# Kernel tuning notes

Measured on AMD Instinct MI355X. Metric: run time of the kernel, lower is better.

## Reference

```python
import jax, jax.numpy as jnp
import numpy as np

B, S, D, HD = 16, 2048, 1024, 64  # batch, seq, n_embd, head_dim


def setup_inputs() -> dict:
    key = jax.random.key(0)
    ks = jax.random.split(key, 4)
    std = 1.0 / np.sqrt(D)
    return {
        "x": jax.random.normal(ks[0], (B, S, D), dtype=jnp.float32),
        "Wq": jax.random.normal(ks[1], (D, HD), dtype=jnp.float32) * std,
        "bq": jnp.zeros((HD,), dtype=jnp.float32),
        "Wk": jax.random.normal(ks[2], (D, HD), dtype=jnp.float32) * std,
        "bk": jnp.zeros((HD,), dtype=jnp.float32),
        "Wv": jax.random.normal(ks[3], (D, HD), dtype=jnp.float32) * std,
        "bv": jnp.zeros((HD,), dtype=jnp.float32),
    }


def reference(x, Wq, bq, Wk, bk, Wv, bv):
    q = x @ Wq + bq  # [B,S,HD]
    k = x @ Wk + bk
    v = x @ Wv + bv
    scale = jnp.asarray(HD, x.dtype) ** -0.5
    scores = jnp.einsum("bqd,bkd->bqk", q, k) * scale  # [B,S,S]
    seq = x.shape[1]
    causal = jnp.tril(jnp.ones((seq, seq), dtype=bool))  # True = keep
    scores = jnp.where(causal, scores, jnp.asarray(-jnp.inf, scores.dtype))
    probs = jax.nn.softmax(scores, axis=-1)
    return jnp.einsum("bqk,bkd->bqd", probs, v)  # [B,S,HD]
```

## Files before the change

### kernel.cpp

```cpp
#include <hip/hip_runtime.h>
#include <hip/hip_bf16.h>
#include <math.h>

constexpr int Bsz  = 16;
constexpr int Seq  = 2048;
constexpr int Din  = 1024;
constexpr int Hd   = 64;
constexpr int Rows = Bsz * Seq;

typedef short  short8 __attribute__((ext_vector_type(8)));
typedef float  f32x4  __attribute__((ext_vector_type(4)));

__device__ __forceinline__ short bf16_bits(float f) {
    __hip_bfloat16 h = __float2bfloat16(f);
    return __builtin_bit_cast(short, h);
}

typedef __attribute__((address_space(1))) const void gvoid_t;
typedef __attribute__((address_space(3))) void lvoid_t;
__device__ __forceinline__ void gll16(const void* g, void* l) {
    __builtin_amdgcn_global_load_lds((gvoid_t*)g, (lvoid_t*)l, 16, 0, 0);
}

__global__ __launch_bounds__(256) void wt_prep(
    const float* __restrict__ Wq, const float* __restrict__ Wk,
    const float* __restrict__ Wv, short* __restrict__ Wf)
{
    const int u     = blockIdx.x * 256 + threadIdx.x;
    const int chunk = u / 768;
    const int rem   = u - chunk * 768;
    const int f     = rem >> 6;
    const int lane  = rem & 63;
    const int wg    = f >> 2, nt = f & 3;
    const int quad  = lane >> 4, l16 = lane & 15;
    const float* W  = (wg == 0) ? Wq : (wg == 1) ? Wk : Wv;
    const int k0 = chunk * 32 + quad * 8;
    const int n  = nt * 16 + l16;
    short8 v;
    #pragma unroll
    for (int j = 0; j < 8; ++j) v[j] = bf16_bits(W[(size_t)(k0 + j) * Hd + n]);
    *(short8*)(Wf + (size_t)u * 8) = v;
}

template<int RD, int ST, bool STAGE, bool PREF>
__device__ __forceinline__ void qkv_step(
    const short*& wf_stage, short* sW, int wave, int lane,
    const float*& xpf,
    float4& a0, float4& a1, float4& b0, float4& b1,
    f32x4 (&acc)[12])
{
    if (STAGE) {
        short* lp = sW + ST * 6144 + wave * 1536;
        gll16(wf_stage,        lp);
        gll16(wf_stage +  512, lp +  512);
        gll16(wf_stage + 1024, lp + 1024);
        wf_stage += 6144;
    }
    asm volatile("" ::: "memory");
    float4 n0, n1;
    if (PREF) {
        n0 = *(const float4*)xpf;
        n1 = *(const float4*)(xpf + 4);
        xpf += 32;
    }
    short8 af;
    af[0] = bf16_bits(a0.x); af[1] = bf16_bits(a0.y);
    af[2] = bf16_bits(a0.z); af[3] = bf16_bits(a0.w);
    af[4] = bf16_bits(a1.x); af[5] = bf16_bits(a1.y);
    af[6] = bf16_bits(a1.z); af[7] = bf16_bits(a1.w);
    const short* wsrc = sW + RD * 6144 + lane * 8;
    #pragma unroll
    for (int f = 0; f < 12; ++f) {
        const short8 bb = *(const short8*)(wsrc + f * 512);
        acc[f] = __builtin_amdgcn_mfma_f32_16x16x32_bf16(af, bb, acc[f], 0, 0, 0);
    }
    a0 = b0; a1 = b1;
    if (PREF) { b0 = n0; b1 = n1; }
}

#define QKV_BAR(N)                                                      \
    asm volatile("s_waitcnt vmcnt(" #N ") lgkmcnt(0)" ::: "memory");    \
    __builtin_amdgcn_s_barrier();

__global__ __launch_bounds__(256) void qkv_kernel(
    const float* __restrict__ x,
    const short* __restrict__ Wf,
    const float* __restrict__ bq, const float* __restrict__ bk,
    const float* __restrict__ bv,
    short* __restrict__ Qf, short* __restrict__ Kf, short* __restrict__ Vf)
{
    const int tid  = threadIdx.x;
    const int wave = tid >> 6;
    const int lane = tid & 63;
    const int quad = lane >> 4;
    const int l16  = lane & 15;
    const int bx   = blockIdx.x;
    const int m0   = bx * 64;

    __shared__ __align__(16) short smem[18432];
    short* sW = smem;

    const float* xrow = x + (size_t)(m0 + wave * 16 + l16) * Din + quad * 8;

    f32x4 acc[12] = {};

    {
        const short* gp = Wf + wave * 1536 + lane * 8;
        short*       lp = sW + wave * 1536;
        gll16(gp,        lp);
        gll16(gp +  512, lp +  512);
        gll16(gp + 1024, lp + 1024);
        const short* gp1 = gp + 6144;
        short*       lp1 = lp + 6144;
        gll16(gp1,        lp1);
        gll16(gp1 +  512, lp1 +  512);
        gll16(gp1 + 1024, lp1 + 1024);
    }
    asm volatile("" ::: "memory");
    float4 a0 = *(const float4*)(xrow);
    float4 a1 = *(const float4*)(xrow + 4);
    float4 b0 = *(const float4*)(xrow + 32);
    float4 b1 = *(const float4*)(xrow + 36);
    QKV_BAR(7)

    const short* wf_stage = Wf + 2 * 6144 + wave * 1536 + lane * 8;
    const float* xpf      = xrow + 2 * 32;

    #pragma unroll 1
    for (int c3 = 0; c3 < 30; c3 += 3) {
        qkv_step<0, 2, true, true>(wf_stage, sW, wave, lane, xpf, a0, a1, b0, b1, acc);
        QKV_BAR(7)
        qkv_step<1, 0, true, true>(wf_stage, sW, wave, lane, xpf, a0, a1, b0, b1, acc);
        QKV_BAR(7)
        qkv_step<2, 1, true, true>(wf_stage, sW, wave, lane, xpf, a0, a1, b0, b1, acc);
        QKV_BAR(7)
    }
    qkv_step<0, 0, false, false>(wf_stage, sW, wave, lane, xpf, a0, a1, b0, b1, acc);
    QKV_BAR(2)
    qkv_step<1, 0, false, false>(wf_stage, sW, wave, lane, xpf, a0, a1, b0, b1, acc);

    __syncthreads();

    short (*eS)[2][16 * 72] = reinterpret_cast<short(*)[2][16 * 72]>(smem);
    short* eV = smem + 9216;

    #pragma unroll
    for (int wg = 0; wg < 2; ++wg) {
        const float* bias = wg ? bk : bq;
        #pragma unroll
        for (int nt = 0; nt < 4; ++nt) {
            const float bb = bias[nt * 16 + l16];
            #pragma unroll
            for (int r = 0; r < 4; ++r)
                eS[wave][wg][(quad * 4 + r) * 72 + nt * 16 + l16] =
                    bf16_bits(acc[wg * 4 + nt][r] + bb);
        }
    }
    #pragma unroll
    for (int wg = 0; wg < 2; ++wg) {
        const short8 v0 = *(const short8*)&eS[wave][wg][l16 * 72 + quad * 8];
        const short8 v1 = *(const short8*)&eS[wave][wg][l16 * 72 + 32 + quad * 8];
        if (wg == 0) {
            const size_t tg = (size_t)bx * 4 + wave;
            *(short8*)(Qf + (tg * 2 + 0) * 512 + lane * 8) = v0;
            *(short8*)(Qf + (tg * 2 + 1) * 512 + lane * 8) = v1;
        } else {
            *(short8*)(Kf + (((size_t)bx * 2 + 0) * 4 + wave) * 512 + lane * 8) = v0;
            *(short8*)(Kf + (((size_t)bx * 2 + 1) * 4 + wave) * 512 + lane * 8) = v1;
        }
    }

    #pragma unroll
    for (int nt = 0; nt < 4; ++nt) {
        const float bb = bv[nt * 16 + l16];
        #pragma unroll
        for (int r = 0; r < 4; ++r)
            eV[(nt * 16 + l16) * 80 + wave * 16 + quad * 4 + r] =
                bf16_bits(acc[8 + nt][r] + bb);
    }
    __syncthreads();
    #pragma unroll
    for (int s = 0; s < 2; ++s) {
        const int slot   = tid + s * 256;
        const int lane_s = slot & 63;
        const int u      = slot >> 6;
        const int th     = u >> 2, ntd = u & 3;
        const int q_s    = lane_s >> 4, l_s = lane_s & 15;
        const short8 v = *(const short8*)&eV[(ntd * 16 + l_s) * 80 + th * 32 + q_s * 8];
        *(short8*)(Vf + (((size_t)bx * 2 + th) * 4 + ntd) * 512 + lane_s * 8) = v;
    }
}

__global__ __launch_bounds__(256) void attn_kernel(
    const short* __restrict__ Qf, const short* __restrict__ Kf,
    const short* __restrict__ Vf, float* __restrict__ out)
{
    const int tid  = threadIdx.x;
    const int wave = tid >> 6;
    const int lane = tid & 63;
    const int quad = lane >> 4;
    const int l16  = lane & 15;
    const int b    = blockIdx.y;
    const int bx   = blockIdx.x;
    const int qs   = (bx & 1) ? (127 - (bx >> 1)) : (bx >> 1);
    const int dTile = qs >> 2;
    const int tiles = dTile + 1;
    const int qoff  = (qs & 3) * 16;

    __shared__ __align__(16) unsigned char sm[17408 + 512];
    short* Ps   = (short*)sm;
    float* Obuf = (float*)sm;
    float* mb   = (float*)(sm + 17408);
    float* lb   = mb + 64;

    const size_t tg = (size_t)b * 128 + qs;
    const short8 qf0 = *(const short8*)(Qf + (tg * 2 + 0) * 512 + lane * 8);
    const short8 qf1 = *(const short8*)(Qf + (tg * 2 + 1) * 512 + lane * 8);

    f32x4 o[4] = {};
    float m_run[4], l_run[4];
    #pragma unroll
    for (int r = 0; r < 4; ++r) { m_run[r] = -INFINITY; l_run[r] = 0.0f; }

    const float C = 0.125f * 1.44269504088896340736f;

    for (int kt = wave; kt < tiles; kt += 4) {
        const short* ktile = Kf + (size_t)(b * 32 + kt) * 4096;
        const short* vtile = Vf + (size_t)(b * 32 + kt) * 4096;

        f32x4 s[4] = {};
        __builtin_amdgcn_s_setprio(1);
        #pragma unroll
        for (int nt = 0; nt < 4; ++nt) {
            const short8 kf0 = *(const short8*)(ktile + ((0 * 4 + nt) * 64 + lane) * 8);
            const short8 kf1 = *(const short8*)(ktile + ((1 * 4 + nt) * 64 + lane) * 8);
            s[nt] = __builtin_amdgcn_mfma_f32_16x16x32_bf16(qf0, kf0, s[nt], 0, 0, 0);
            s[nt] = __builtin_amdgcn_mfma_f32_16x16x32_bf16(qf1, kf1, s[nt], 0, 0, 0);
        }
        __builtin_amdgcn_s_setprio(0);

        if (kt == dTile) {
            #pragma unroll
            for (int nt = 0; nt < 4; ++nt) {
                const int kg = nt * 16 + l16;
                #pragma unroll
                for (int r = 0; r < 4; ++r) {
                    const int qg = qoff + quad * 4 + r;
                    s[nt][r] = (kg <= qg) ? s[nt][r] * C : -INFINITY;
                }
            }
        } else {
            #pragma unroll
            for (int nt = 0; nt < 4; ++nt)
                #pragma unroll
                for (int r = 0; r < 4; ++r) s[nt][r] *= C;
        }

        float rm[4];
        #pragma unroll
        for (int r = 0; r < 4; ++r)
            rm[r] = fmaxf(fmaxf(s[0][r], s[1][r]), fmaxf(s[2][r], s[3][r]));
        #pragma unroll
        for (int off = 1; off < 16; off <<= 1)
            #pragma unroll
            for (int r = 0; r < 4; ++r)
                rm[r] = fmaxf(rm[r], __shfl_xor(rm[r], off));

        float alpha[4];
        #pragma unroll
        for (int r = 0; r < 4; ++r) {
            const float mn = fmaxf(m_run[r], rm[r]);
            alpha[r] = exp2f(m_run[r] - mn);
            m_run[r] = mn;
        }

        float rs[4] = {0.f, 0.f, 0.f, 0.f};
        #pragma unroll
        for (int nt = 0; nt < 4; ++nt)
            #pragma unroll
            for (int r = 0; r < 4; ++r) {
                const float p = exp2f(s[nt][r] - m_run[r]);
                s[nt][r] = p;
                rs[r] += p;
            }
        #pragma unroll
        for (int off = 1; off < 16; off <<= 1)
            #pragma unroll
            for (int r = 0; r < 4; ++r)
                rs[r] += __shfl_xor(rs[r], off);
        #pragma unroll
        for (int r = 0; r < 4; ++r) l_run[r] = l_run[r] * alpha[r] + rs[r];

        #pragma unroll
        for (int r = 0; r < 4; ++r) {
            o[0][r] *= alpha[r]; o[1][r] *= alpha[r];
            o[2][r] *= alpha[r]; o[3][r] *= alpha[r];
        }

        #pragma unroll
        for (int nt = 0; nt < 4; ++nt)
            #pragma unroll
            for (int r = 0; r < 4; ++r)
                Ps[wave * 1152 + (quad * 4 + r) * 72 + nt * 16 + l16] = bf16_bits(s[nt][r]);

        const short8 pf0 = *(const short8*)&Ps[wave * 1152 + l16 * 72 + quad * 8];
        const short8 pf1 = *(const short8*)&Ps[wave * 1152 + l16 * 72 + 32 + quad * 8];

        __builtin_amdgcn_s_setprio(1);
        #pragma unroll
        for (int nt = 0; nt < 4; ++nt) {
            const short8 vA = *(const short8*)(vtile + ((0 * 4 + nt) * 64 + lane) * 8);
            const short8 vB = *(const short8*)(vtile + ((1 * 4 + nt) * 64 + lane) * 8);
            o[nt] = __builtin_amdgcn_mfma_f32_16x16x32_bf16(pf0, vA, o[nt], 0, 0, 0);
            o[nt] = __builtin_amdgcn_mfma_f32_16x16x32_bf16(pf1, vB, o[nt], 0, 0, 0);
        }
        __builtin_amdgcn_s_setprio(0);
    }

    if (l16 == 0) {
        #pragma unroll
        for (int r = 0; r < 4; ++r) mb[wave * 16 + quad * 4 + r] = m_run[r];
    }
    __syncthreads();

    float fac[4];
    #pragma unroll
    for (int r = 0; r < 4; ++r) {
        const int row = quad * 4 + r;
        const float mg = fmaxf(fmaxf(mb[row], mb[16 + row]),
                               fmaxf(mb[32 + row], mb[48 + row]));
        fac[r] = exp2f(m_run[r] - mg);
    }
    if (l16 == 0) {
        #pragma unroll
        for (int r = 0; r < 4; ++r) lb[wave * 16 + quad * 4 + r] = l_run[r] * fac[r];
    }
    #pragma unroll
    for (int nt = 0; nt < 4; ++nt)
        #pragma unroll
        for (int r = 0; r < 4; ++r)
            Obuf[wave * 1088 + (quad * 4 + r) * 68 + nt * 16 + l16] = o[nt][r] * fac[r];
    __syncthreads();

    {
        const int row = tid >> 4;
        const int c0  = (tid & 15) * 4;
        const float lsum = lb[row] + lb[16 + row] + lb[32 + row] + lb[48 + row];
        float4 a = *(const float4*)&Obuf[0 * 1088 + row * 68 + c0];
        const float4 a1 = *(const float4*)&Obuf[1 * 1088 + row * 68 + c0];
        const float4 a2 = *(const float4*)&Obuf[2 * 1088 + row * 68 + c0];
        const float4 a3 = *(const float4*)&Obuf[3 * 1088 + row * 68 + c0];
        a.x += a1.x + a2.x + a3.x;  a.y += a1.y + a2.y + a3.y;
        a.z += a1.z + a2.z + a3.z;  a.w += a1.w + a2.w + a3.w;
        const float inv = 1.0f / lsum;
        float4 r4 = make_float4(a.x * inv, a.y * inv, a.z * inv, a.w * inv);
        *(float4*)(out + ((size_t)b * Seq + qs * 16 + row) * Hd + c0) = r4;
    }
}

extern "C" void kernel_launch(void* const* d_in, const int* in_sizes, int n_in,
                              void* d_out, int out_size, void* d_ws, size_t ws_size,
                              hipStream_t stream)
{
    const float* x  = (const float*)d_in[0];
    const float* Wq = (const float*)d_in[1];
    const float* bq = (const float*)d_in[2];
    const float* Wk = (const float*)d_in[3];
    const float* bk = (const float*)d_in[4];
    const float* Wv = (const float*)d_in[5];
    const float* bv = (const float*)d_in[6];
    float* out = (float*)d_out;

    short* Qf = (short*)d_ws;
    short* Kf = Qf + (size_t)Rows * Hd;
    short* Vf = Kf + (size_t)Rows * Hd;
    short* Wf = Vf + (size_t)Rows * Hd;

    wt_prep<<<96, 256, 0, stream>>>(Wq, Wk, Wv, Wf);
    qkv_kernel<<<512, 256, 0, stream>>>(x, Wf, bq, bk, bv, Qf, Kf, Vf);
    attn_kernel<<<dim3(128, 16), 256, 0, stream>>>(Qf, Kf, Vf, out);
}
```

Baseline: 275.3 us.

## Share double-buffered K/V tiles in LDS across waves handling 64 query rows

```diff
diff --git a/kernel.cpp b/kernel.cpp
--- a/kernel.cpp
+++ b/kernel.cpp
@@ -202,21 +202,23 @@
     const int l16  = lane & 15;
     const int b    = blockIdx.y;
     const int bx   = blockIdx.x;
-    const int qs   = (bx & 1) ? (127 - (bx >> 1)) : (bx >> 1);
-    const int dTile = qs >> 2;
-    const int tiles = dTile + 1;
-    const int qoff  = (qs & 3) * 16;
-
-    __shared__ __align__(16) unsigned char sm[17408 + 512];
-    short* Ps   = (short*)sm;
-    float* Obuf = (float*)sm;
-    float* mb   = (float*)(sm + 17408);
-    float* lb   = mb + 64;
+    const int qb0  = (bx & 1) ? (31 - (bx >> 1)) : (bx >> 1);
+    const int qb   = (blockIdx.y & 8) ? (31 - qb0) : qb0;
+    const int ntiles = qb + 1;
+    const int qs   = qb * 4 + wave;
+    const int qoff = wave * 16;
+
+    __shared__ __align__(16) short kv[2][8192];
+    __shared__ __align__(16) short Ps[4][1152];
+    float* Obuf = (float*)kv;
 
     const size_t tg = (size_t)b * 128 + qs;
     const short8 qf0 = *(const short8*)(Qf + (tg * 2 + 0) * 512 + lane * 8);
     const short8 qf1 = *(const short8*)(Qf + (tg * 2 + 1) * 512 + lane * 8);
 
+    const short* kbase = Kf + (size_t)b * 32 * 4096;
+    const short* vbase = Vf + (size_t)b * 32 * 4096;
+
     f32x4 o[4] = {};
     float m_run[4], l_run[4];
     #pragma unroll
@@ -224,9 +226,32 @@
 
     const float C = 0.125f * 1.44269504088896340736f;
 
-    for (int kt = wave; kt < tiles; kt += 4) {
-        const short* ktile = Kf + (size_t)(b * 32 + kt) * 4096;
-        const short* vtile = Vf + (size_t)(b * 32 + kt) * 4096;
+    {
+        const short* gk = kbase + wave * 1024 + lane * 8;
+        const short* gv = vbase + wave * 1024 + lane * 8;
+        short* lk = &kv[0][0]    + wave * 1024;
+        short* lv = &kv[0][4096] + wave * 1024;
+        gll16(gk,       lk);
+        gll16(gk + 512, lk + 512);
+        gll16(gv,       lv);
+        gll16(gv + 512, lv + 512);
+    }
+    __syncthreads();
+
+    for (int kt = 0; kt < ntiles; ++kt) {
+        const int cur = kt & 1;
+        if (kt + 1 < ntiles) {
+            const short* gk = kbase + (size_t)(kt + 1) * 4096 + wave * 1024 + lane * 8;
+            const short* gv = vbase + (size_t)(kt + 1) * 4096 + wave * 1024 + lane * 8;
+            short* lk = &kv[cur ^ 1][0]    + wave * 1024;
+            short* lv = &kv[cur ^ 1][4096] + wave * 1024;
+            gll16(gk,       lk);
+            gll16(gk + 512, lk + 512);
+            gll16(gv,       lv);
+            gll16(gv + 512, lv + 512);
+        }
+        const short* ktile = &kv[cur][0];
+        const short* vtile = &kv[cur][4096];
 
         f32x4 s[4] = {};
         __builtin_amdgcn_s_setprio(1);
@@ -239,7 +264,7 @@
         }
         __builtin_amdgcn_s_setprio(0);
 
-        if (kt == dTile) {
+        if (kt == qb) {
             #pragma unroll
             for (int nt = 0; nt < 4; ++nt) {
                 const int kg = nt * 16 + l16;
@@ -301,10 +326,10 @@
         for (int nt = 0; nt < 4; ++nt)
             #pragma unroll
             for (int r = 0; r < 4; ++r)
-                Ps[wave * 1152 + (quad * 4 + r) * 72 + nt * 16 + l16] = bf16_bits(s[nt][r]);
-
-        const short8 pf0 = *(const short8*)&Ps[wave * 1152 + l16 * 72 + quad * 8];
-        const short8 pf1 = *(const short8*)&Ps[wave * 1152 + l16 * 72 + 32 + quad * 8];
+                Ps[wave][(quad * 4 + r) * 72 + nt * 16 + l16] = bf16_bits(s[nt][r]);
+
+        const short8 pf0 = *(const short8*)&Ps[wave][l16 * 72 + quad * 8];
+        const short8 pf1 = *(const short8*)&Ps[wave][l16 * 72 + 32 + quad * 8];
 
         __builtin_amdgcn_s_setprio(1);
         #pragma unroll
@@ -315,46 +340,26 @@
             o[nt] = __builtin_amdgcn_mfma_f32_16x16x32_bf16(pf1, vB, o[nt], 0, 0, 0);
         }
         __builtin_amdgcn_s_setprio(0);
-    }
-
-    if (l16 == 0) {
-        #pragma unroll
-        for (int r = 0; r < 4; ++r) mb[wave * 16 + quad * 4 + r] = m_run[r];
-    }
-    __syncthreads();
-
-    float fac[4];
-    #pragma unroll
-    for (int r = 0; r < 4; ++r) {
-        const int row = quad * 4 + r;
-        const float mg = fmaxf(fmaxf(mb[row], mb[16 + row]),
-                               fmaxf(mb[32 + row], mb[48 + row]));
-        fac[r] = exp2f(m_run[r] - mg);
-    }
-    if (l16 == 0) {
-        #pragma unroll
-        for (int r = 0; r < 4; ++r) lb[wave * 16 + quad * 4 + r] = l_run[r] * fac[r];
-    }
+
+        __syncthreads();
+    }
+
+    float inv[4];
+    #pragma unroll
+    for (int r = 0; r < 4; ++r) inv[r] = 1.0f / l_run[r];
     #pragma unroll
     for (int nt = 0; nt < 4; ++nt)
         #pragma unroll
         for (int r = 0; r < 4; ++r)
-            Obuf[wave * 1088 + (quad * 4 + r) * 68 + nt * 16 + l16] = o[nt][r] * fac[r];
-    __syncthreads();
-
+            Obuf[wave * 1088 + (quad * 4 + r) * 68 + nt * 16 + l16] = o[nt][r] * inv[r];
     {
-        const int row = tid >> 4;
-        const int c0  = (tid & 15) * 4;
-        const float lsum = lb[row] + lb[16 + row] + lb[32 + row] + lb[48 + row];
-        float4 a = *(const float4*)&Obuf[0 * 1088 + row * 68 + c0];
-        const float4 a1 = *(const float4*)&Obuf[1 * 1088 + row * 68 + c0];
-        const float4 a2 = *(const float4*)&Obuf[2 * 1088 + row * 68 + c0];
-        const float4 a3 = *(const float4*)&Obuf[3 * 1088 + row * 68 + c0];
-        a.x += a1.x + a2.x + a3.x;  a.y += a1.y + a2.y + a3.y;
-        a.z += a1.z + a2.z + a3.z;  a.w += a1.w + a2.w + a3.w;
-        const float inv = 1.0f / lsum;
-        float4 r4 = make_float4(a.x * inv, a.y * inv, a.z * inv, a.w * inv);
-        *(float4*)(out + ((size_t)b * Seq + qs * 16 + row) * Hd + c0) = r4;
+        const int row = lane >> 2;
+        const int c0  = (lane & 3) * 16;
+        float* dst = out + ((size_t)b * Seq + (size_t)qs * 16 + row) * Hd + c0;
+        const float* src = &Obuf[wave * 1088 + row * 68 + c0];
+        #pragma unroll
+        for (int j = 0; j < 4; ++j)
+            *(float4*)(dst + j * 4) = *(const float4*)(src + j * 4);
     }
 }
 
@@ -378,5 +383,5 @@
 
     wt_prep<<<96, 256, 0, stream>>>(Wq, Wk, Wv, Wf);
     qkv_kernel<<<512, 256, 0, stream>>>(x, Wf, bq, bk, bv, Qf, Kf, Vf);
-    attn_kernel<<<dim3(128, 16), 256, 0, stream>>>(Qf, Kf, Vf, out);
-}
+    attn_kernel<<<dim3(32, 16), 256, 0, stream>>>(Qf, Kf, Vf, out);
+}
```

New measurement: 273.5 us. About the same (-0.6%).
